# Kernel optimization log

Measured on AMD Instinct MI355X. Metric: run time of the kernel, lower is better.

The kernel has to match this reference:

```python
import jax, jax.numpy as jnp
import numpy as np

FACTOR = 2  # self.factor
KSIZE = 3   # causal_fusion depthwise conv kernel size


def causal_fusion(x, w, b):
    # x: [BH, C, N]; depthwise causal conv over the node axis (left pad k-1)
    k = w.shape[-1]
    out = jax.lax.conv_general_dilated(
        x, w, window_strides=(1,), padding=[(k - 1, 0)],
        dimension_numbers=('NCH', 'OIH', 'NCH'),
        feature_group_count=x.shape[1])
    return out + b[None, :, None]


def setup_inputs() -> dict:
    key = jax.random.key(0)
    ks = jax.random.split(key, 4)
    B, N, L, H, E = 4, 64, 128, 8, 32
    queries = jax.random.normal(ks[0], (B, N, L, H, E), jnp.float32)
    keys = jax.random.normal(ks[1], (B, N, L, H, E), jnp.float32)
    values = jax.random.normal(ks[2], (B, N, L, H, E), jnp.float32)
    attn_mask = jnp.zeros((1,), jnp.bool_)
    C = E * L  # 4096 channels seen by causal_fusion
    w_cf = jax.random.normal(ks[3], (C, 1, KSIZE), jnp.float32) * 0.05
    b_cf = jnp.zeros((C,), jnp.float32)
    return {"queries": queries, "keys": keys, "values": values,
            "attn_mask": attn_mask, "w_cf": w_cf, "b_cf": b_cf}


def reference(queries, keys, values, attn_mask, w_cf, b_cf):
    B, N, L, H, E = queries.shape  # S == L, so no pad/slice branch taken

    # --- FFT cross-correlation: corr[b,n,h,e,:] = irfft(rfft(mean_n q) * conj(rfft(k)))
    qm = jnp.broadcast_to(jnp.mean(queries, axis=1, keepdims=True), queries.shape)
    qp = jnp.transpose(qm, (0, 1, 3, 4, 2))      # [B,N,H,E,L]
    kp = jnp.transpose(keys, (0, 1, 3, 4, 2))    # [B,N,H,E,L]
    vp = jnp.transpose(values, (0, 1, 3, 4, 2))  # [B,N,H,E,L]
    corr = jnp.fft.irfft(jnp.fft.rfft(qp, axis=-1) * jnp.conj(jnp.fft.rfft(kp, axis=-1)), n=L, axis=-1)

    # --- align_speed: top-k delays over channel-mean corr, circular roll of values
    mean_corr = jnp.mean(corr, axis=3)                      # [B,N,H,L]
    weight, delay_idx = jax.lax.top_k(mean_corr, FACTOR)    # [B,N,H,F]
    delay = L - delay_idx                                   # values in [1, L]
    ar = jnp.arange(L)
    aligned = []
    for i in range(FACTOR):
        idx = (ar[None, None, None, None, :] + delay[..., i][..., None, None]) % L  # [B,N,H,1,L]
        idx = jnp.broadcast_to(idx, vp.shape)
        aligned.append(jnp.take_along_axis(vp, idx, axis=-1))  # [B,N,H,E,L]

    BH = B * H
    delay_bh = jnp.transpose(delay, (0, 2, 1, 3)).reshape(BH, N, FACTOR)
    weight_bh = jnp.transpose(weight, (0, 2, 1, 3)).reshape(BH, N, FACTOR)

    # --- per-factor: sort nodes by delay -> causal fusion over nodes -> unsort
    causal_agg = []
    for i in range(FACTOR):
        indices = jnp.argsort(delay_bh[..., i], axis=-1)               # [BH,N]
        av = jnp.transpose(aligned[i], (0, 2, 1, 3, 4)).reshape(BH, N, E, L)
        av = av * jax.nn.sigmoid(weight_bh[..., i])[:, :, None, None]
        sorted_av = jnp.take_along_axis(av, indices[:, :, None, None], axis=1)
        x = jnp.transpose(sorted_av.reshape(BH, N, E * L), (0, 2, 1))  # [BH,E*L,N]
        x = causal_fusion(x, w_cf, b_cf)
        x = jnp.transpose(x, (0, 2, 1)).reshape(BH, N, E, L)
        rev = jnp.argsort(indices, axis=-1)
        x = jnp.take_along_axis(x, rev[:, :, None, None], axis=1)
        causal_agg.append(jnp.transpose(x.reshape(B, H, N, E, L), (0, 2, 1, 3, 4)))  # [B,N,H,E,L]

    # --- align_back_speed: inverse circular shift, mean over factors
    delay_back = L - delay  # [B,N,H,F]
    agg = jnp.zeros_like(causal_agg[0])
    for i in range(FACTOR):
        idx = (ar[None, None, None, None, :] + delay_back[..., i][..., None, None]) % L
        idx = jnp.broadcast_to(idx, causal_agg[i].shape)
        agg = agg + jnp.take_along_axis(causal_agg[i], idx, axis=-1)
    agg = agg / FACTOR

    V = jnp.transpose(agg, (0, 1, 4, 2, 3))  # [B,N,L,H,E]
    return V
```

## Files before the change

### kernel.cpp

```cpp
#include <hip/hip_runtime.h>
#include <math.h>

#define B_ 4
#define N_ 64
#define L_ 128
#define H_ 8
#define E_ 32
#define SC_ 8

typedef __attribute__((ext_vector_type(8))) short short8;
typedef __attribute__((ext_vector_type(4))) float f32x4;
typedef __attribute__((ext_vector_type(4))) _Float16 f16x4;

__device__ __forceinline__ unsigned short f2bf(float x) {
    union { float f; unsigned u; } c; c.f = x;
    unsigned r = (c.u + 0x7fffu + ((c.u >> 16) & 1u)) >> 16;
    return (unsigned short)r;
}
__device__ __forceinline__ float bf2f(unsigned short h) {
    union { unsigned u; float f; } c; c.u = ((unsigned)h) << 16;
    return c.f;
}

__global__ __launch_bounds__(256) void k_qmean(const float* __restrict__ q,
                                               float* __restrict__ qm,
                                               const float* __restrict__ w,
                                               const float* __restrict__ bias,
                                               _Float16* __restrict__ wTh,
                                               _Float16* __restrict__ bTh,
                                               int* __restrict__ wcnt) {
    int blk = blockIdx.x;
    int b = blk >> 7, t = blk & 127;
    int tid = threadIdx.x;
    int c4 = tid & 63;
    int nq = tid >> 6;
    __shared__ double red[4][256];
    const f32x4* p = (const f32x4*)(q + (((size_t)(b * N_)) * L_ + t) * 256);
    double s0 = 0, s1 = 0, s2 = 0, s3 = 0;
    #pragma unroll 4
    for (int n = nq * 16; n < nq * 16 + 16; ++n) {
        f32x4 v = p[(size_t)n * 8192 + c4];
        s0 += (double)v.x; s1 += (double)v.y; s2 += (double)v.z; s3 += (double)v.w;
    }
    red[nq][c4 * 4 + 0] = s0;
    red[nq][c4 * 4 + 1] = s1;
    red[nq][c4 * 4 + 2] = s2;
    red[nq][c4 * 4 + 3] = s3;
    __syncthreads();
    int c = tid;
    double s = red[0][c] + red[1][c] + red[2][c] + red[3][c];
    qm[((size_t)b * 256 + c) * L_ + t] = (float)(s * (1.0 / 64.0));

    if (blk < 16) {
        int k = blk * 256 + tid;
        int e = k & 31, lp = k >> 5;
        int cc = e * L_ + lp;
        wTh[k]        = (_Float16)w[cc * 3 + 0];
        wTh[4096 + k] = (_Float16)w[cc * 3 + 1];
        wTh[8192 + k] = (_Float16)w[cc * 3 + 2];
        bTh[k]        = (_Float16)bias[cc];
    }
    if (blk == 16 && tid == 0) *wcnt = 0;
}

__global__ __launch_bounds__(512) void k_corr(const float* __restrict__ keys,
                                              const float* __restrict__ qm,
                                              float* __restrict__ part) {
    int blk = blockIdx.x;
    int sc = blk & 7; int bh = blk >> 3; int h = bh & 7; int b = bh >> 3;
    __shared__ unsigned short Ahi[4][64][40];
    __shared__ unsigned short Alo[4][64][40];
    __shared__ unsigned short Qhi[128][40];
    __shared__ unsigned short Qlo[128][40];
    int tid = threadIdx.x;
    int lane = tid & 63, w = tid >> 6;
    int mg = w & 1, ng = w >> 1;

    {
        int e = tid >> 4; int tq = (tid & 15) * 4;
        const float* qp = qm + ((size_t)b * 256 + h * 32 + e) * 128;
        #pragma unroll
        for (int hf = 0; hf < 2; ++hf) {
            int t0 = tq + hf * 64;
            float4 v = *(const float4*)(qp + t0);
            float vv[4] = {v.x, v.y, v.z, v.w};
            #pragma unroll
            for (int j = 0; j < 4; ++j) {
                unsigned short hi = f2bf(vv[j]);
                Qhi[t0 + j][e] = hi;
                Qlo[t0 + j][e] = f2bf(vv[j] - bf2f(hi));
            }
        }
    }
    int sn = tid >> 3; int se = (tid & 7) * 4;
    const float* kbase = keys + ((size_t)(b * N_ + sn) * L_) * 256 + h * 32 + se;
    #pragma unroll
    for (int p = 0; p < 2; ++p) {
        float4 v = *(const float4*)(kbase + (size_t)(sc * 16 + p) * 256);
        float vv[4] = {v.x, v.y, v.z, v.w};
        ushort4 h4, l4;
        unsigned short* hp = (unsigned short*)&h4;
        unsigned short* lp = (unsigned short*)&l4;
        #pragma unroll
        for (int j = 0; j < 4; ++j) {
            hp[j] = f2bf(vv[j]);
            lp[j] = f2bf(vv[j] - bf2f(hp[j]));
        }
        *(ushort4*)&Ahi[p][sn][se] = h4;
        *(ushort4*)&Alo[p][sn][se] = l4;
    }
    __syncthreads();

    f32x4 acc[2][2];
    #pragma unroll
    for (int i = 0; i < 2; ++i)
        #pragma unroll
        for (int j = 0; j < 2; ++j)
            acc[i][j] = (f32x4){0.f, 0.f, 0.f, 0.f};

    int eb = (lane >> 4) * 8;
    int rA0 = (mg * 2) * 16 + (lane & 15);
    int rA1 = rA0 + 16;
    int tau0 = (ng * 2) * 16 + (lane & 15);
    int tau1 = tau0 + 16;

    for (int it = 0; it < 8; ++it) {
        float4 stg0, stg1;
        if (it < 7) {
            stg0 = *(const float4*)(kbase + (size_t)(sc * 16 + 2 * it + 2) * 256);
            stg1 = *(const float4*)(kbase + (size_t)(sc * 16 + 2 * it + 3) * 256);
        }
        #pragma unroll
        for (int sp = 0; sp < 2; ++sp) {
            int p = 2 * it + sp;
            int slot = p & 3;
            int s = sc * 16 + p;
            short8 ah0 = *(const short8*)&Ahi[slot][rA0][eb];
            short8 ah1 = *(const short8*)&Ahi[slot][rA1][eb];
            short8 al0 = *(const short8*)&Alo[slot][rA0][eb];
            short8 al1 = *(const short8*)&Alo[slot][rA1][eb];
            int t0 = (s + tau0) & 127;
            int t1 = (s + tau1) & 127;
            short8 bh0 = *(const short8*)&Qhi[t0][eb];
            short8 bh1 = *(const short8*)&Qhi[t1][eb];
            short8 bl0 = *(const short8*)&Qlo[t0][eb];
            short8 bl1 = *(const short8*)&Qlo[t1][eb];
            acc[0][0] = __builtin_amdgcn_mfma_f32_16x16x32_bf16(ah0, bh0, acc[0][0], 0, 0, 0);
            acc[0][1] = __builtin_amdgcn_mfma_f32_16x16x32_bf16(ah0, bh1, acc[0][1], 0, 0, 0);
            acc[1][0] = __builtin_amdgcn_mfma_f32_16x16x32_bf16(ah1, bh0, acc[1][0], 0, 0, 0);
            acc[1][1] = __builtin_amdgcn_mfma_f32_16x16x32_bf16(ah1, bh1, acc[1][1], 0, 0, 0);
            acc[0][0] = __builtin_amdgcn_mfma_f32_16x16x32_bf16(ah0, bl0, acc[0][0], 0, 0, 0);
            acc[0][1] = __builtin_amdgcn_mfma_f32_16x16x32_bf16(ah0, bl1, acc[0][1], 0, 0, 0);
            acc[1][0] = __builtin_amdgcn_mfma_f32_16x16x32_bf16(ah1, bl0, acc[1][0], 0, 0, 0);
            acc[1][1] = __builtin_amdgcn_mfma_f32_16x16x32_bf16(ah1, bl1, acc[1][1], 0, 0, 0);
            acc[0][0] = __builtin_amdgcn_mfma_f32_16x16x32_bf16(al0, bh0, acc[0][0], 0, 0, 0);
            acc[0][1] = __builtin_amdgcn_mfma_f32_16x16x32_bf16(al0, bh1, acc[0][1], 0, 0, 0);
            acc[1][0] = __builtin_amdgcn_mfma_f32_16x16x32_bf16(al1, bh0, acc[1][0], 0, 0, 0);
            acc[1][1] = __builtin_amdgcn_mfma_f32_16x16x32_bf16(al1, bh1, acc[1][1], 0, 0, 0);
        }
        if (it < 7) {
            #pragma unroll
            for (int sp = 0; sp < 2; ++sp) {
                int p = 2 * it + 2 + sp;
                int slot = p & 3;
                float4 v = sp ? stg1 : stg0;
                float vv[4] = {v.x, v.y, v.z, v.w};
                ushort4 h4, l4;
                unsigned short* hp = (unsigned short*)&h4;
                unsigned short* lp = (unsigned short*)&l4;
                #pragma unroll
                for (int j = 0; j < 4; ++j) {
                    hp[j] = f2bf(vv[j]);
                    lp[j] = f2bf(vv[j] - bf2f(hp[j]));
                }
                *(ushort4*)&Ahi[slot][sn][se] = h4;
                *(ushort4*)&Alo[slot][sn][se] = l4;
            }
        }
        __syncthreads();
    }

    #pragma unroll
    for (int i = 0; i < 2; ++i) {
        int mt = mg * 2 + i;
        #pragma unroll
        for (int j = 0; j < 2; ++j) {
            int nt = ng * 2 + j;
            int tau = nt * 16 + (lane & 15);
            #pragma unroll
            for (int r = 0; r < 4; ++r) {
                int n = mt * 16 + (lane >> 4) * 4 + r;
                part[((((size_t)sc * B_ + b) * N_ + n) * H_ + h) * L_ + tau] = acc[i][j][r];
            }
        }
    }
}

__global__ __launch_bounds__(256) void k_topk(const float* __restrict__ part,
                                              int* __restrict__ didx,
                                              float* __restrict__ sig,
                                              int* __restrict__ flags,
                                              int* __restrict__ wlist,
                                              int* __restrict__ wcnt) {
    int blk = blockIdx.x * 4 + (threadIdx.x >> 6);
    int lane = threadIdx.x & 63;
    size_t rb = (size_t)blk * L_;
    const size_t stride = (size_t)B_ * N_ * H_ * L_;
    double s0 = 0.0, s1 = 0.0;
    for (int sc = 0; sc < SC_; ++sc) {
        s0 += (double)part[sc * stride + rb + lane];
        s1 += (double)part[sc * stride + rb + lane + 64];
    }
    float v0 = (float)(s0 * (1.0 / 32.0));
    float v1 = (float)(s1 * (1.0 / 32.0));

    float bv = v0; int bi = lane;
    if (v1 > v0) { bv = v1; bi = lane + 64; }
    #pragma unroll
    for (int m = 32; m; m >>= 1) {
        float ov = __shfl_xor(bv, m, 64);
        int   oi = __shfl_xor(bi, m, 64);
        if (ov > bv || (ov == bv && oi < bi)) { bv = ov; bi = oi; }
    }
    int i1 = bi; float w1v = bv;

    float c0 = (lane == i1) ? -INFINITY : v0;
    float c1 = (lane + 64 == i1) ? -INFINITY : v1;
    float bv2 = c0; int bi2 = lane;
    if (c1 > c0) { bv2 = c1; bi2 = lane + 64; }
    #pragma unroll
    for (int m = 32; m; m >>= 1) {
        float ov = __shfl_xor(bv2, m, 64);
        int   oi = __shfl_xor(bi2, m, 64);
        if (ov > bv2 || (ov == bv2 && oi < bi2)) { bv2 = ov; bi2 = oi; }
    }
    int i2 = bi2; float w2v = bv2;

    float d0 = (lane == i1 || lane == i2) ? -INFINITY : v0;
    float d1 = (lane + 64 == i1 || lane + 64 == i2) ? -INFINITY : v1;
    float bv3 = fmaxf(d0, d1);
    #pragma unroll
    for (int m = 32; m; m >>= 1) bv3 = fmaxf(bv3, __shfl_xor(bv3, m, 64));

    if (lane == 0) {
        didx[blk * 2 + 0] = i1;
        didx[blk * 2 + 1] = i2;
        sig[blk * 2 + 0] = 1.f / (1.f + expf(-w1v));
        sig[blk * 2 + 1] = 1.f / (1.f + expf(-w2v));
        int fl = (w2v - bv3 < 1e-3f) ? 1 : 0;
        flags[blk] = fl;
        if (fl) { int s = atomicAdd(wcnt, 1); wlist[s] = blk; }
    }
}

__global__ __launch_bounds__(256) void k_fixup(const float* __restrict__ keys,
                                               const float* __restrict__ qm,
                                               const int* __restrict__ wlist,
                                               const int* __restrict__ wcnt,
                                               double* __restrict__ vvg) {
    int cnt = *wcnt;
    __shared__ float ks_t[L_][E_];
    __shared__ float qs_t[L_][E_];
    __shared__ double red[16][17];
    int tid = threadIdx.x;
    for (int wi = blockIdx.x; wi < cnt * 8; wi += gridDim.x) {
        int row = wlist[wi >> 3]; int tg = wi & 7;
        int h = row & 7; int r = row >> 3; int n = r & 63; int b = r >> 6;
        __syncthreads();
        for (int idx = tid; idx < 1024; idx += 256) {
            int s = idx >> 3, e4 = idx & 7;
            *(float4*)&ks_t[s][e4 * 4] =
                *(const float4*)&keys[(((size_t)(b * N_ + n)) * L_ + s) * 256 + h * E_ + e4 * 4];
            int e = idx >> 5, t4 = (idx & 31) * 4;
            float4 v = *(const float4*)&qm[((size_t)b * 256 + h * E_ + e) * L_ + t4];
            float vvj[4] = {v.x, v.y, v.z, v.w};
            #pragma unroll
            for (int j = 0; j < 4; ++j) {
                int t = t4 + j;
                int col = ((((e >> 2) ^ (t & 7)) << 2) | (e & 3));
                qs_t[t][col] = vvj[j];
            }
        }
        __syncthreads();
        int tau = tg * 16 + (tid & 15);
        int g = tid >> 4;
        double a0 = 0, a1 = 0, a2 = 0, a3 = 0, a4 = 0, a5 = 0, a6 = 0, a7 = 0;
        #pragma unroll 2
        for (int s = g * 8; s < g * 8 + 8; ++s) {
            int t = (s + tau) & 127;
            int x = t & 7;
            #pragma unroll
            for (int e4 = 0; e4 < 8; e4 += 2) {
                float4 k0 = *(const float4*)&ks_t[s][e4 * 4];
                float4 k1 = *(const float4*)&ks_t[s][e4 * 4 + 4];
                float4 q0 = *(const float4*)&qs_t[t][(e4 ^ x) << 2];
                float4 q1 = *(const float4*)&qs_t[t][((e4 + 1) ^ x) << 2];
                a0 = fma((double)k0.x, (double)q0.x, a0);
                a1 = fma((double)k0.y, (double)q0.y, a1);
                a2 = fma((double)k0.z, (double)q0.z, a2);
                a3 = fma((double)k0.w, (double)q0.w, a3);
                a4 = fma((double)k1.x, (double)q1.x, a4);
                a5 = fma((double)k1.y, (double)q1.y, a5);
                a6 = fma((double)k1.z, (double)q1.z, a6);
                a7 = fma((double)k1.w, (double)q1.w, a7);
            }
        }
        red[g][tid & 15] = ((a0 + a1) + (a2 + a3)) + ((a4 + a5) + (a6 + a7));
        __syncthreads();
        if (tid < 16) {
            double s = 0;
            #pragma unroll
            for (int gg = 0; gg < 16; ++gg) s += red[gg][tid];
            vvg[(size_t)row * L_ + tg * 16 + tid] = s;
        }
    }
}

__global__ __launch_bounds__(128) void k_sort(const int* __restrict__ didx,
                                              const float* __restrict__ sig,
                                              const int* __restrict__ flags,
                                              const double* __restrict__ vvg,
                                              int4* __restrict__ gparam_i,
                                              f32x4* __restrict__ gparam_f) {
    int bh = blockIdx.x;
    int b = bh >> 3, h = bh & 7;
    int tid = threadIdx.x; int i = tid >> 6; int n = tid & 63;
    __shared__ int ds[2][64];
    __shared__ int pm[2][64];
    __shared__ int dival[2][64];
    __shared__ float sigval[2][64];
    {
        int row = (b * 64 + n) * 8 + h;
        int dv = didx[row * 2 + i];
        dival[i][n] = dv;
        sigval[i][n] = sig[row * 2 + i];
        ds[i][n] = 128 - dv;
    }
    __syncthreads();

    if (tid < 64) {
        int lane = tid;
        int myflag = flags[(b * 64 + lane) * 8 + h];
        unsigned long long msk = __ballot(myflag != 0);
        while (msk) {
            int nn = __ffsll((long long)msk) - 1; msk &= msk - 1;
            int row = (b * 64 + nn) * 8 + h;
            float v0 = (float)(vvg[(size_t)row * L_ + lane] * (1.0 / 32.0));
            float v1 = (float)(vvg[(size_t)row * L_ + lane + 64] * (1.0 / 32.0));
            float bv = v0; int bi = lane;
            if (v1 > v0) { bv = v1; bi = lane + 64; }
            #pragma unroll
            for (int m = 32; m; m >>= 1) {
                float ov = __shfl_xor(bv, m, 64);
                int   oi = __shfl_xor(bi, m, 64);
                if (ov > bv || (ov == bv && oi < bi)) { bv = ov; bi = oi; }
            }
            int i1 = bi; float w1v = bv;
            float c0 = (lane == i1) ? -INFINITY : v0;
            float c1 = (lane + 64 == i1) ? -INFINITY : v1;
            float bv2 = c0; int bi2 = lane;
            if (c1 > c0) { bv2 = c1; bi2 = lane + 64; }
            #pragma unroll
            for (int m = 32; m; m >>= 1) {
                float ov = __shfl_xor(bv2, m, 64);
                int   oi = __shfl_xor(bi2, m, 64);
                if (ov > bv2 || (ov == bv2 && oi < bi2)) { bv2 = ov; bi2 = oi; }
            }
            if (lane == 0) {
                dival[0][nn] = i1;      ds[0][nn] = 128 - i1;
                dival[1][nn] = bi2;     ds[1][nn] = 128 - bi2;
                sigval[0][nn] = 1.f / (1.f + expf(-w1v));
                sigval[1][nn] = 1.f / (1.f + expf(-bv2));
            }
        }
    }
    __syncthreads();

    int d = ds[i][n];
    int rank = 0;
    for (int m = 0; m < 64; ++m) {
        int dm = ds[i][m];
        rank += (dm < d || (dm == d && m < n)) ? 1 : 0;
    }
    pm[i][rank] = n;
    __syncthreads();
    int p1v = (rank >= 1) ? pm[i][rank - 1] : -1;
    int p2v = (rank >= 2) ? pm[i][rank - 2] : -1;

    int din = dival[i][n];
    int pq1 = (p1v >= 0) ? p1v : n;
    int pq2 = (p2v >= 0) ? p2v : n;
    int d1 = (p1v >= 0) ? ((din - dival[i][p1v]) & 127) : 0;
    int d2 = (p2v >= 0) ? ((din - dival[i][p2v]) & 127) : 0;
    float s1 = (p1v >= 0) ? sigval[i][p1v] : 0.f;
    float s2 = (p2v >= 0) ? sigval[i][p2v] : 0.f;
    int blko = (b * 64 + n) * 8 + h;
    gparam_i[blko * 2 + i] = make_int4(pq1, pq2, d1, d2);
    gparam_f[blko * 2 + i] = (f32x4){s1, s2, sigval[i][n], (float)din};
}

__global__ __launch_bounds__(256, 3) void k_out(const float* __restrict__ values,
                                                const _Float16* __restrict__ wTh,
                                                const _Float16* __restrict__ bTh,
                                                const int4* __restrict__ gparam_i,
                                                const f32x4* __restrict__ gparam_f,
                                                float* __restrict__ out) {
    int bid = blockIdx.x;
    int h = bid & 7;
    int q = (bid >> 3) & 3;
    int n = (bid >> 5) & 63;
    int b = bid >> 11;
    int blk = (b * 64 + n) * 8 + h;
    int tid = threadIdx.x; int e4 = tid & 7; int tq = tid >> 3;
    int t = q * 32 + tq;

    int4  gi0 = gparam_i[blk * 2 + 0];
    int4  gi1 = gparam_i[blk * 2 + 1];
    f32x4 gf0 = gparam_f[blk * 2 + 0];
    f32x4 gf1 = gparam_f[blk * 2 + 1];
    int di0 = (int)gf0.w, di1 = (int)gf1.w;

    const f32x4* v4 = (const f32x4*)values;
    const f16x4* w4 = (const f16x4*)wTh;
    const f16x4* b4 = (const f16x4*)bTh;
    f32x4* o4 = (f32x4*)out;
    const size_t base = ((size_t)b * N_) * L_ * 64 + h * 8 + e4;

    f32x4 vs  = v4[base + ((size_t)n * L_ + t) * 64];
    f32x4 va1 = v4[base + ((size_t)gi0.x * L_ + ((t + gi0.z) & 127)) * 64];
    f32x4 va2 = v4[base + ((size_t)gi0.y * L_ + ((t + gi0.w) & 127)) * 64];
    f32x4 vb1 = v4[base + ((size_t)gi1.x * L_ + ((t + gi1.z) & 127)) * 64];
    f32x4 vb2 = v4[base + ((size_t)gi1.y * L_ + ((t + gi1.w) & 127)) * 64];
    int wo0 = ((t + di0) & 127) * 8 + e4;
    int wo1 = ((t + di1) & 127) * 8 + e4;
    f32x4 bb0 = __builtin_convertvector(b4[wo0], f32x4);
    f32x4 w0a = __builtin_convertvector(w4[wo0], f32x4);
    f32x4 w1a = __builtin_convertvector(w4[1024 + wo0], f32x4);
    f32x4 w2a = __builtin_convertvector(w4[2048 + wo0], f32x4);
    f32x4 bb1 = __builtin_convertvector(b4[wo1], f32x4);
    f32x4 w0b = __builtin_convertvector(w4[wo1], f32x4);
    f32x4 w1b = __builtin_convertvector(w4[1024 + wo1], f32x4);
    f32x4 w2b = __builtin_convertvector(w4[2048 + wo1], f32x4);

    f32x4 acc = bb0 + bb1;
    acc += w2a * (gf0.z * vs);
    acc += w1a * (gf0.x * va1);
    acc += w0a * (gf0.y * va2);
    acc += w2b * (gf1.z * vs);
    acc += w1b * (gf1.x * vb1);
    acc += w0b * (gf1.y * vb2);
    acc *= 0.5f;
    __builtin_nontemporal_store(acc, &o4[base + ((size_t)n * L_ + t) * 64]);
}

extern "C" void kernel_launch(void* const* d_in, const int* in_sizes, int n_in,
                              void* d_out, int out_size, void* d_ws, size_t ws_size,
                              hipStream_t stream) {
    const float* queries = (const float*)d_in[0];
    const float* keys    = (const float*)d_in[1];
    const float* values  = (const float*)d_in[2];
    const float* w_cf = (const float*)d_in[4];
    const float* b_cf = (const float*)d_in[5];
    float* out = (float*)d_out;

    float* ws    = (float*)d_ws;
    float*    qm  = ws;
    _Float16* wTh = (_Float16*)(qm + 131072);
    _Float16* bTh = wTh + 12288;
    float*  sigp  = (float*)(bTh + 4096);
    int*   didxp = (int*)(sigp + 4096);
    int*   flags = didxp + 4096;
    int*   wlist = flags + 2048;
    int*   wcnt  = wlist + 2048;
    double* vvg  = (double*)(wcnt + 4);
    int4*  gpi   = (int4*)(vvg + 2048 * 128);
    f32x4* gpf   = (f32x4*)(gpi + 4096);

    float* part = (float*)d_out;

    k_qmean <<<512,  256, 0, stream>>>(queries, qm, w_cf, b_cf, wTh, bTh, wcnt);
    k_corr  <<<256,  512, 0, stream>>>(keys, qm, part);
    k_topk  <<<512,  256, 0, stream>>>(part, didxp, sigp, flags, wlist, wcnt);
    k_fixup <<<256,  256, 0, stream>>>(keys, qm, wlist, wcnt, vvg);
    k_sort  <<<32,   128, 0, stream>>>(didxp, sigp, flags, vvg, gpi, gpf);
    k_out   <<<8192, 256, 0, stream>>>(values, wTh, bTh, gpi, gpf, out);
}
```

Baseline: 70.32 us.

## Fuse near-tie fp64 fixup and re-topk into top-k kernel

Merges the fixup kernel (fp64 recompute of ambiguous correlation rows) into the top-k kernel. Each block now recomputes its own flagged rows locally and redoes the top-2 selection in place. This drops a kernel launch, the atomic worklist, the fp64 global buffer and the flag handling in the sort kernel. The cost is that each flagged row is now processed serially by a single 256-thread block over all 128 lags, instead of being spread across 8 blocks. Blocks holding flagged rows may therefore become stragglers.

```diff
diff --git a/kernel.cpp b/kernel.cpp
--- a/kernel.cpp
+++ b/kernel.cpp
@@ -27,8 +27,7 @@
                                                const float* __restrict__ w,
                                                const float* __restrict__ bias,
                                                _Float16* __restrict__ wTh,
-                                               _Float16* __restrict__ bTh,
-                                               int* __restrict__ wcnt) {
+                                               _Float16* __restrict__ bTh) {
     int blk = blockIdx.x;
     int b = blk >> 7, t = blk & 127;
     int tid = threadIdx.x;
@@ -60,7 +59,6 @@
         wTh[8192 + k] = (_Float16)w[cc * 3 + 2];
         bTh[k]        = (_Float16)bias[cc];
     }
-    if (blk == 16 && tid == 0) *wcnt = 0;
 }
 
 __global__ __launch_bounds__(512) void k_corr(const float* __restrict__ keys,
@@ -197,76 +195,73 @@
 }
 
 __global__ __launch_bounds__(256) void k_topk(const float* __restrict__ part,
+                                              const float* __restrict__ keys,
+                                              const float* __restrict__ qm,
                                               int* __restrict__ didx,
-                                              float* __restrict__ sig,
-                                              int* __restrict__ flags,
-                                              int* __restrict__ wlist,
-                                              int* __restrict__ wcnt) {
-    int blk = blockIdx.x * 4 + (threadIdx.x >> 6);
-    int lane = threadIdx.x & 63;
-    size_t rb = (size_t)blk * L_;
-    const size_t stride = (size_t)B_ * N_ * H_ * L_;
-    double s0 = 0.0, s1 = 0.0;
-    for (int sc = 0; sc < SC_; ++sc) {
-        s0 += (double)part[sc * stride + rb + lane];
-        s1 += (double)part[sc * stride + rb + lane + 64];
-    }
-    float v0 = (float)(s0 * (1.0 / 32.0));
-    float v1 = (float)(s1 * (1.0 / 32.0));
-
-    float bv = v0; int bi = lane;
-    if (v1 > v0) { bv = v1; bi = lane + 64; }
-    #pragma unroll
-    for (int m = 32; m; m >>= 1) {
-        float ov = __shfl_xor(bv, m, 64);
-        int   oi = __shfl_xor(bi, m, 64);
-        if (ov > bv || (ov == bv && oi < bi)) { bv = ov; bi = oi; }
-    }
-    int i1 = bi; float w1v = bv;
-
-    float c0 = (lane == i1) ? -INFINITY : v0;
-    float c1 = (lane + 64 == i1) ? -INFINITY : v1;
-    float bv2 = c0; int bi2 = lane;
-    if (c1 > c0) { bv2 = c1; bi2 = lane + 64; }
-    #pragma unroll
-    for (int m = 32; m; m >>= 1) {
-        float ov = __shfl_xor(bv2, m, 64);
-        int   oi = __shfl_xor(bi2, m, 64);
-        if (ov > bv2 || (ov == bv2 && oi < bi2)) { bv2 = ov; bi2 = oi; }
-    }
-    int i2 = bi2; float w2v = bv2;
-
-    float d0 = (lane == i1 || lane == i2) ? -INFINITY : v0;
-    float d1 = (lane + 64 == i1 || lane + 64 == i2) ? -INFINITY : v1;
-    float bv3 = fmaxf(d0, d1);
-    #pragma unroll
-    for (int m = 32; m; m >>= 1) bv3 = fmaxf(bv3, __shfl_xor(bv3, m, 64));
-
-    if (lane == 0) {
-        didx[blk * 2 + 0] = i1;
-        didx[blk * 2 + 1] = i2;
-        sig[blk * 2 + 0] = 1.f / (1.f + expf(-w1v));
-        sig[blk * 2 + 1] = 1.f / (1.f + expf(-w2v));
-        int fl = (w2v - bv3 < 1e-3f) ? 1 : 0;
-        flags[blk] = fl;
-        if (fl) { int s = atomicAdd(wcnt, 1); wlist[s] = blk; }
-    }
-}
-
-__global__ __launch_bounds__(256) void k_fixup(const float* __restrict__ keys,
-                                               const float* __restrict__ qm,
-                                               const int* __restrict__ wlist,
-                                               const int* __restrict__ wcnt,
-                                               double* __restrict__ vvg) {
-    int cnt = *wcnt;
+                                              float* __restrict__ sig) {
+    int bid = blockIdx.x;
+    int tid = threadIdx.x;
+    int w = tid >> 6, lane = tid & 63;
     __shared__ float ks_t[L_][E_];
     __shared__ float qs_t[L_][E_];
-    __shared__ double red[16][17];
-    int tid = threadIdx.x;
-    for (int wi = blockIdx.x; wi < cnt * 8; wi += gridDim.x) {
-        int row = wlist[wi >> 3]; int tg = wi & 7;
-        int h = row & 7; int r = row >> 3; int n = r & 63; int b = r >> 6;
-        __syncthreads();
+    __shared__ double vvL[2][L_];
+    __shared__ int   dA[4][2];
+    __shared__ float sA[4][2];
+    __shared__ int   flagL[4];
+
+    {
+        int blk = bid * 4 + w;
+        size_t rb = (size_t)blk * L_;
+        const size_t stride = (size_t)B_ * N_ * H_ * L_;
+        double s0 = 0.0, s1 = 0.0;
+        for (int sc = 0; sc < SC_; ++sc) {
+            s0 += (double)part[sc * stride + rb + lane];
+            s1 += (double)part[sc * stride + rb + lane + 64];
+        }
+        float v0 = (float)(s0 * (1.0 / 32.0));
+        float v1 = (float)(s1 * (1.0 / 32.0));
+
+        float bv = v0; int bi = lane;
+        if (v1 > v0) { bv = v1; bi = lane + 64; }
+        #pragma unroll
+        for (int m = 32; m; m >>= 1) {
+            float ov = __shfl_xor(bv, m, 64);
+            int   oi = __shfl_xor(bi, m, 64);
+            if (ov > bv || (ov == bv && oi < bi)) { bv = ov; bi = oi; }
+        }
+        int i1 = bi; float w1v = bv;
+
+        float c0 = (lane == i1) ? -INFINITY : v0;
+        float c1 = (lane + 64 == i1) ? -INFINITY : v1;
+        float bv2 = c0; int bi2 = lane;
+        if (c1 > c0) { bv2 = c1; bi2 = lane + 64; }
+        #pragma unroll
+        for (int m = 32; m; m >>= 1) {
+            float ov = __shfl_xor(bv2, m, 64);
+            int   oi = __shfl_xor(bi2, m, 64);
+            if (ov > bv2 || (ov == bv2 && oi < bi2)) { bv2 = ov; bi2 = oi; }
+        }
+        int i2 = bi2; float w2v = bv2;
+
+        float d0 = (lane == i1 || lane == i2) ? -INFINITY : v0;
+        float d1 = (lane + 64 == i1 || lane + 64 == i2) ? -INFINITY : v1;
+        float bv3 = fmaxf(d0, d1);
+        #pragma unroll
+        for (int m = 32; m; m >>= 1) bv3 = fmaxf(bv3, __shfl_xor(bv3, m, 64));
+
+        if (lane == 0) {
+            dA[w][0] = i1; dA[w][1] = i2;
+            sA[w][0] = 1.f / (1.f + expf(-w1v));
+            sA[w][1] = 1.f / (1.f + expf(-w2v));
+            flagL[w] = (w2v - bv3 < 1e-3f) ? 1 : 0;
+        }
+    }
+    __syncthreads();
+
+    for (int r = 0; r < 4; ++r) {
+        if (!flagL[r]) continue;
+        int rblk = bid * 4 + r;
+        int h = rblk & 7; int rr = rblk >> 3; int n = rr & 63; int b = rr >> 6;
         for (int idx = tid; idx < 1024; idx += 256) {
             int s = idx >> 3, e4 = idx & 7;
             *(float4*)&ks_t[s][e4 * 4] =
@@ -282,19 +277,18 @@
             }
         }
         __syncthreads();
-        int tau = tg * 16 + (tid & 15);
-        int g = tid >> 4;
+        int tau = tid & 127, hf = tid >> 7;
         double a0 = 0, a1 = 0, a2 = 0, a3 = 0, a4 = 0, a5 = 0, a6 = 0, a7 = 0;
-        #pragma unroll 2
-        for (int s = g * 8; s < g * 8 + 8; ++s) {
+        for (int s = 0; s < L_; ++s) {
             int t = (s + tau) & 127;
             int x = t & 7;
             #pragma unroll
-            for (int e4 = 0; e4 < 8; e4 += 2) {
-                float4 k0 = *(const float4*)&ks_t[s][e4 * 4];
-                float4 k1 = *(const float4*)&ks_t[s][e4 * 4 + 4];
-                float4 q0 = *(const float4*)&qs_t[t][(e4 ^ x) << 2];
-                float4 q1 = *(const float4*)&qs_t[t][((e4 + 1) ^ x) << 2];
+            for (int g = 0; g < 4; g += 2) {
+                int g0 = hf * 4 + g;
+                float4 k0 = *(const float4*)&ks_t[s][g0 * 4];
+                float4 k1 = *(const float4*)&ks_t[s][g0 * 4 + 4];
+                float4 q0 = *(const float4*)&qs_t[t][(g0 ^ x) << 2];
+                float4 q1 = *(const float4*)&qs_t[t][((g0 + 1) ^ x) << 2];
                 a0 = fma((double)k0.x, (double)q0.x, a0);
                 a1 = fma((double)k0.y, (double)q0.y, a1);
                 a2 = fma((double)k0.z, (double)q0.z, a2);
@@ -305,21 +299,49 @@
                 a7 = fma((double)k1.w, (double)q1.w, a7);
             }
         }
-        red[g][tid & 15] = ((a0 + a1) + (a2 + a3)) + ((a4 + a5) + (a6 + a7));
+        vvL[hf][tau] = ((a0 + a1) + (a2 + a3)) + ((a4 + a5) + (a6 + a7));
         __syncthreads();
-        if (tid < 16) {
-            double s = 0;
-            #pragma unroll
-            for (int gg = 0; gg < 16; ++gg) s += red[gg][tid];
-            vvg[(size_t)row * L_ + tg * 16 + tid] = s;
-        }
+        if (tid < 64) {
+            float v0 = (float)((vvL[0][lane] + vvL[1][lane]) * (1.0 / 32.0));
+            float v1 = (float)((vvL[0][lane + 64] + vvL[1][lane + 64]) * (1.0 / 32.0));
+            float bv = v0; int bi = lane;
+            if (v1 > v0) { bv = v1; bi = lane + 64; }
+            #pragma unroll
+            for (int m = 32; m; m >>= 1) {
+                float ov = __shfl_xor(bv, m, 64);
+                int   oi = __shfl_xor(bi, m, 64);
+                if (ov > bv || (ov == bv && oi < bi)) { bv = ov; bi = oi; }
+            }
+            int i1 = bi; float w1v = bv;
+            float c0 = (lane == i1) ? -INFINITY : v0;
+            float c1 = (lane + 64 == i1) ? -INFINITY : v1;
+            float bv2 = c0; int bi2 = lane;
+            if (c1 > c0) { bv2 = c1; bi2 = lane + 64; }
+            #pragma unroll
+            for (int m = 32; m; m >>= 1) {
+                float ov = __shfl_xor(bv2, m, 64);
+                int   oi = __shfl_xor(bi2, m, 64);
+                if (ov > bv2 || (ov == bv2 && oi < bi2)) { bv2 = ov; bi2 = oi; }
+            }
+            if (lane == 0) {
+                dA[r][0] = i1; dA[r][1] = bi2;
+                sA[r][0] = 1.f / (1.f + expf(-w1v));
+                sA[r][1] = 1.f / (1.f + expf(-bv2));
+            }
+        }
+        __syncthreads();
+    }
+
+    if (tid < 8) {
+        int rw = tid >> 1, i = tid & 1;
+        int row = bid * 4 + rw;
+        didx[row * 2 + i] = dA[rw][i];
+        sig[row * 2 + i]  = sA[rw][i];
     }
 }
 
 __global__ __launch_bounds__(128) void k_sort(const int* __restrict__ didx,
                                               const float* __restrict__ sig,
-                                              const int* __restrict__ flags,
-                                              const double* __restrict__ vvg,
                                               int4* __restrict__ gparam_i,
                                               f32x4* __restrict__ gparam_f) {
     int bh = blockIdx.x;
@@ -338,44 +360,6 @@
     }
     __syncthreads();
 
-    if (tid < 64) {
-        int lane = tid;
-        int myflag = flags[(b * 64 + lane) * 8 + h];
-        unsigned long long msk = __ballot(myflag != 0);
-        while (msk) {
-            int nn = __ffsll((long long)msk) - 1; msk &= msk - 1;
-            int row = (b * 64 + nn) * 8 + h;
-            float v0 = (float)(vvg[(size_t)row * L_ + lane] * (1.0 / 32.0));
-            float v1 = (float)(vvg[(size_t)row * L_ + lane + 64] * (1.0 / 32.0));
-            float bv = v0; int bi = lane;
-            if (v1 > v0) { bv = v1; bi = lane + 64; }
-            #pragma unroll
-            for (int m = 32; m; m >>= 1) {
-                float ov = __shfl_xor(bv, m, 64);
-                int   oi = __shfl_xor(bi, m, 64);
-                if (ov > bv || (ov == bv && oi < bi)) { bv = ov; bi = oi; }
-            }
-            int i1 = bi; float w1v = bv;
-            float c0 = (lane == i1) ? -INFINITY : v0;
-            float c1 = (lane + 64 == i1) ? -INFINITY : v1;
-            float bv2 = c0; int bi2 = lane;
-            if (c1 > c0) { bv2 = c1; bi2 = lane + 64; }
-            #pragma unroll
-            for (int m = 32; m; m >>= 1) {
-                float ov = __shfl_xor(bv2, m, 64);
-                int   oi = __shfl_xor(bi2, m, 64);
-                if (ov > bv2 || (ov == bv2 && oi < bi2)) { bv2 = ov; bi2 = oi; }
-            }
-            if (lane == 0) {
-                dival[0][nn] = i1;      ds[0][nn] = 128 - i1;
-                dival[1][nn] = bi2;     ds[1][nn] = 128 - bi2;
-                sigval[0][nn] = 1.f / (1.f + expf(-w1v));
-                sigval[1][nn] = 1.f / (1.f + expf(-bv2));
-            }
-        }
-    }
-    __syncthreads();
-
     int d = ds[i][n];
     int rank = 0;
     for (int m = 0; m < 64; ++m) {
@@ -469,19 +453,14 @@
     _Float16* bTh = wTh + 12288;
     float*  sigp  = (float*)(bTh + 4096);
     int*   didxp = (int*)(sigp + 4096);
-    int*   flags = didxp + 4096;
-    int*   wlist = flags + 2048;
-    int*   wcnt  = wlist + 2048;
-    double* vvg  = (double*)(wcnt + 4);
-    int4*  gpi   = (int4*)(vvg + 2048 * 128);
+    int4*  gpi   = (int4*)(didxp + 4096);
     f32x4* gpf   = (f32x4*)(gpi + 4096);
 
     float* part = (float*)d_out;
 
-    k_qmean <<<512,  256, 0, stream>>>(queries, qm, w_cf, b_cf, wTh, bTh, wcnt);
+    k_qmean <<<512,  256, 0, stream>>>(queries, qm, w_cf, b_cf, wTh, bTh);
     k_corr  <<<256,  512, 0, stream>>>(keys, qm, part);
-    k_topk  <<<512,  256, 0, stream>>>(part, didxp, sigp, flags, wlist, wcnt);
-    k_fixup <<<256,  256, 0, stream>>>(keys, qm, wlist, wcnt, vvg);
-    k_sort  <<<32,   128, 0, stream>>>(didxp, sigp, flags, vvg, gpi, gpf);
+    k_topk  <<<512,  256, 0, stream>>>(part, keys, qm, didxp, sigp);
+    k_sort  <<<32,   128, 0, stream>>>(didxp, sigp, gpi, gpf);
     k_out   <<<8192, 256, 0, stream>>>(values, wTh, bTh, gpi, gpf, out);
 }
```

Measured after the change: 100.6 us. +43.1%, slower.
